# Kernel optimization log

Measured on AMD Instinct MI355X. Metric: run time of the kernel, lower is better.

The kernel has to match this reference:

```python
import jax, jax.numpy as jnp
import numpy as np

B, CIN, COUT, KH, KW, H, W = 32, 64, 64, 3, 3, 128, 128
STRIDE = (1, 1)
PADDING = [(1, 1), (1, 1)]


def setup_inputs() -> dict:
    key = jax.random.key(0)
    k1, k2, k3, k4 = jax.random.split(key, 4)
    x = jax.random.normal(k1, (B, CIN, H, W), dtype=jnp.float32)
    cov = jax.random.uniform(k2, (B,), dtype=jnp.float32)
    # kaiming-normal fan_out init: std = sqrt(2 / (cout*kh*kw))
    std = np.sqrt(2.0 / (COUT * KH * KW)).astype(np.float32)
    W_0 = jax.random.normal(k3, (COUT, CIN, KH, KW), dtype=jnp.float32) * std
    W_1 = jax.random.normal(k4, (COUT, CIN, KH, KW), dtype=jnp.float32) * std
    return {"x": x, "cov": cov, "W_0": W_0, "W_1": W_1}


def reference(x, cov, W_0, W_1):
    # per-sample kernel: W_0 + cov[i] * W_1  -> [B, COUT, CIN, KH, KW]
    kernels = W_0[None] + cov[:, None, None, None, None] * W_1[None]

    def conv_one(xi, k):
        # xi: [CIN, H, W], k: [COUT, CIN, KH, KW]
        out = jax.lax.conv_general_dilated(
            xi[None], k, window_strides=STRIDE, padding=PADDING,
            dimension_numbers=("NCHW", "OIHW", "NCHW"))
        return out[0]

    return jax.vmap(conv_one)(x, kernels)  # [B, COUT, H, W]
```

## Files before the change

### kernel.cpp

```cpp
#include <hip/hip_runtime.h>
#include <stdint.h>

#define B_   32
#define CIN  64
#define COUT 64
#define H_   128
#define W_   128
#define WP   130
#define HW_  (H_ * W_)
#define SLOT (WP * 64)

typedef __bf16 bf16x8 __attribute__((ext_vector_type(8)));
typedef float  f32x4  __attribute__((ext_vector_type(4)));

__device__ inline unsigned int f2bf(float f) {
  union { float f; unsigned u; } uf; uf.f = f;
  unsigned u = uf.u;
  unsigned r = 0x7FFFu + ((u >> 16) & 1u);
  return (u + r) >> 16;
}

__device__ inline unsigned int pk2(float a, float b) {
  unsigned short x = __builtin_bit_cast(unsigned short, (__bf16)a);
  unsigned short y = __builtin_bit_cast(unsigned short, (__bf16)b);
  return (unsigned int)x | ((unsigned int)y << 16);
}

__global__ __launch_bounds__(256) void prep_w(const float* __restrict__ W0,
                                              const float* __restrict__ W1,
                                              const float* __restrict__ cov,
                                              unsigned short* __restrict__ Wb) {
  int g   = blockIdx.x * 256 + threadIdx.x;
  int j   = g & 7;
  int l   = (g >> 3) & 63;
  int cq4 = (g >> 9) & 3;
  int ck  = (g >> 11) & 1;
  int v   = g >> 12;
  int b   = v / 9;
  int p   = v - b * 9;
  int cout = cq4 * 16 + (l & 15);
  int ci   = ck * 32 + (l >> 4) * 8 + j;
  int widx = (cout * CIN + ci) * 9 + p;
  float val = W0[widx] + cov[b] * W1[widx];
  Wb[g] = (unsigned short)f2bf(val);
}

__global__ __launch_bounds__(1024, 4) void conv_strip(
    const float* __restrict__ X,
    const unsigned short* __restrict__ Wb,
    float* __restrict__ out) {
  __shared__ __align__(16) unsigned short Xs[6 * SLOT];

  int bid   = blockIdx.x;
  int b     = (bid & 7) * 4 + (bid >> 6);
  int strip = (bid >> 3) & 7;
  int h0    = strip * 16;

  int t  = threadIdx.x;
  int wv = t >> 6;
  int l  = t & 63;
  int lh = l & 15;
  int q  = l >> 4;

  int a = wv >> 3;
  int o = wv & 7;
  int cq4 = wv & 3;
  int pq  = wv >> 2;
  int rbase  = pq >> 1;
  int cbase0 = (pq & 1) * 64 + lh;

  int wp0 = 2 * l + 1, wp1 = 2 * l + 2;
  int sw0 = (o ^ (wp0 & 7)) << 3, sw1 = (o ^ (wp1 & 7)) << 3;

  if (wv < 6) {
    unsigned int* d32 = (unsigned int*)(Xs + wv * SLOT + (l < 32 ? 0 : 129 * 64));
    d32[l & 31] = 0u;
  }
  {
    int r  = wv >> 2;
    int ih = h0 - 1 + r;
    unsigned short* dr = Xs + r * SLOT;
    #pragma unroll
    for (int oi = 0; oi < 2; oi++) {
      int oo = (wv & 3) * 2 + oi;
      uint4 v0 = {0, 0, 0, 0}, v1 = {0, 0, 0, 0};
      if (ih >= 0) {
        const float* sp = X + ((size_t)(b * CIN + oo * 8) * H_ + ih) * W_ + 2 * l;
        float2 tt[8];
        #pragma unroll
        for (int j = 0; j < 8; j++) tt[j] = *(const float2*)(sp + (size_t)j * HW_);
        v0.x = pk2(tt[0].x, tt[1].x); v0.y = pk2(tt[2].x, tt[3].x);
        v0.z = pk2(tt[4].x, tt[5].x); v0.w = pk2(tt[6].x, tt[7].x);
        v1.x = pk2(tt[0].y, tt[1].y); v1.y = pk2(tt[2].y, tt[3].y);
        v1.z = pk2(tt[4].y, tt[5].y); v1.w = pk2(tt[6].y, tt[7].y);
      }
      *(uint4*)(dr + wp0 * 64 + ((oo ^ (wp0 & 7)) << 3)) = v0;
      *(uint4*)(dr + wp1 * 64 + ((oo ^ (wp1 & 7)) << 3)) = v1;
    }
  }
  __syncthreads();

  const unsigned short* wb9 = Wb + (size_t)b * 9 * 4096;

  float2 st[8];
  int sb = 0;

  #pragma unroll 1
  for (int k = 0; k < 8; k++) {
    if (k > 0) {
      int sw = sb + 2 + a; if (sw >= 6) sw -= 6;
      unsigned short* dr = Xs + sw * SLOT;
      uint4 v0, v1;
      v0.x = pk2(st[0].x, st[1].x); v0.y = pk2(st[2].x, st[3].x);
      v0.z = pk2(st[4].x, st[5].x); v0.w = pk2(st[6].x, st[7].x);
      v1.x = pk2(st[0].y, st[1].y); v1.y = pk2(st[2].y, st[3].y);
      v1.z = pk2(st[4].y, st[5].y); v1.w = pk2(st[6].y, st[7].y);
      *(uint4*)(dr + wp0 * 64 + sw0) = v0;
      *(uint4*)(dr + wp1 * 64 + sw1) = v1;
    }
    asm volatile("s_waitcnt lgkmcnt(0)" ::: "memory");
    __builtin_amdgcn_s_barrier();
    __builtin_amdgcn_sched_barrier(0);

    if (k < 7) {
      int ih = h0 + 2 * k + 3 + a;
      if (ih <= 127) {
        const float* sp = X + ((size_t)(b * CIN + o * 8) * H_ + ih) * W_ + 2 * l;
        #pragma unroll
        for (int j = 0; j < 8; j++) st[j] = *(const float2*)(sp + (size_t)j * HW_);
      } else {
        #pragma unroll
        for (int j = 0; j < 8; j++) st[j] = (float2){0.f, 0.f};
      }
    }
    __builtin_amdgcn_sched_barrier(0);

    f32x4 acc[4];
    #pragma unroll
    for (int nt = 0; nt < 4; nt++) acc[nt] = (f32x4){0.f, 0.f, 0.f, 0.f};

    #pragma unroll 1
    for (int kh = 0; kh < 3; kh++) {
      int r6 = sb + rbase + kh; if (r6 >= 6) r6 -= 6;
      const unsigned short* rp = Xs + r6 * SLOT;
      #pragma unroll
      for (int kw = 0; kw < 3; kw++) {
        const unsigned short* wk = wb9 + (kh * 3 + kw) * 4096;
        #pragma unroll
        for (int ck = 0; ck < 2; ck++) {
          bf16x8 af = *(const bf16x8*)(wk + (ck * 4 + cq4) * 512 + l * 8);
          bf16x8 bfr[4];
          #pragma unroll
          for (int nt = 0; nt < 4; nt++) {
            int c = cbase0 + nt * 16 + kw;
            int blk = (ck * 4 + q) ^ (c & 7);
            bfr[nt] = *(const bf16x8*)(rp + c * 64 + blk * 8);
          }
          __builtin_amdgcn_s_setprio(1);
          #pragma unroll
          for (int nt = 0; nt < 4; nt++)
            acc[nt] = __builtin_amdgcn_mfma_f32_16x16x32_bf16(
                af, bfr[nt], acc[nt], 0, 0, 0);
          __builtin_amdgcn_s_setprio(0);
        }
      }
    }

    int oh = h0 + 2 * k + rbase;
    #pragma unroll
    for (int nt = 0; nt < 4; nt++) {
      int ow = cbase0 + nt * 16;
      #pragma unroll
      for (int r = 0; r < 4; r++) {
        int cout = cq4 * 16 + q * 4 + r;
        out[(((size_t)b * COUT + cout) * H_ + oh) * W_ + ow] = acc[nt][r];
      }
    }

    sb += 2; if (sb >= 6) sb -= 6;
  }
}

extern "C" void kernel_launch(void* const* d_in, const int* in_sizes, int n_in,
                              void* d_out, int out_size, void* d_ws, size_t ws_size,
                              hipStream_t stream) {
  const float* x   = (const float*)d_in[0];
  const float* cov = (const float*)d_in[1];
  const float* W0  = (const float*)d_in[2];
  const float* W1  = (const float*)d_in[3];
  float* out = (float*)d_out;

  unsigned short* Wb = (unsigned short*)d_ws;

  prep_w    <<<dim3(4608), dim3(256),  0, stream>>>(W0, W1, cov, Wb);
  conv_strip<<<dim3(256),  dim3(1024), 0, stream>>>(x, Wb, out);
}
```

Measured before the change: 284.7 us.

## Switch conv inner product from 16x16x32 to 32x32x16 bf16 MFMA tiles

Each wave now computes a 32-cout by 32-pixel tile with the 32x32x16 bf16 MFMA instead of four 16x16x32 MFMAs over a 16-cout by 64-pixel tile. The weight prep kernel is relaid out to match the new A-fragment layout, and the output store mapping is changed to fit the 32x32 accumulator layout. The aim is higher MFMA throughput per instruction and fewer B-fragment LDS reads per MAC. In exchange, the accumulator is now sixteen registers per lane and each lane's stores touch more cout rows.

```diff
diff --git a/kernel.cpp b/kernel.cpp
--- a/kernel.cpp
+++ b/kernel.cpp
@@ -11,7 +11,7 @@
 #define SLOT (WP * 64)
 
 typedef __bf16 bf16x8 __attribute__((ext_vector_type(8)));
-typedef float  f32x4  __attribute__((ext_vector_type(4)));
+typedef float  f32x16 __attribute__((ext_vector_type(16)));
 
 __device__ inline unsigned int f2bf(float f) {
   union { float f; unsigned u; } uf; uf.f = f;
@@ -30,16 +30,16 @@
                                               const float* __restrict__ W1,
                                               const float* __restrict__ cov,
                                               unsigned short* __restrict__ Wb) {
-  int g   = blockIdx.x * 256 + threadIdx.x;
-  int j   = g & 7;
-  int l   = (g >> 3) & 63;
-  int cq4 = (g >> 9) & 3;
-  int ck  = (g >> 11) & 1;
-  int v   = g >> 12;
-  int b   = v / 9;
-  int p   = v - b * 9;
-  int cout = cq4 * 16 + (l & 15);
-  int ci   = ck * 32 + (l >> 4) * 8 + j;
+  int g    = blockIdx.x * 256 + threadIdx.x;
+  int j    = g & 7;
+  int l    = (g >> 3) & 63;
+  int ch   = (g >> 9) & 1;
+  int ck16 = (g >> 10) & 3;
+  int v    = g >> 12;
+  int b    = v / 9;
+  int p    = v - b * 9;
+  int cout = ch * 32 + (l & 31);
+  int ci   = ck16 * 16 + (l >> 5) * 8 + j;
   int widx = (cout * CIN + ci) * 9 + p;
   float val = W0[widx] + cov[b] * W1[widx];
   Wb[g] = (unsigned short)f2bf(val);
@@ -59,15 +59,14 @@
   int t  = threadIdx.x;
   int wv = t >> 6;
   int l  = t & 63;
-  int lh = l & 15;
-  int q  = l >> 4;
 
   int a = wv >> 3;
   int o = wv & 7;
-  int cq4 = wv & 3;
-  int pq  = wv >> 2;
-  int rbase  = pq >> 1;
-  int cbase0 = (pq & 1) * 64 + lh;
+  int ch = wv & 1;
+  int pq = wv >> 1;
+  int rbase = pq >> 2;
+  int cpix  = (pq & 3) * 32 + (l & 31);
+  int ohalf = l >> 5;
 
   int wp0 = 2 * l + 1, wp1 = 2 * l + 2;
   int sw0 = (o ^ (wp0 & 7)) << 3, sw1 = (o ^ (wp1 & 7)) << 3;
@@ -135,9 +134,9 @@
     }
     __builtin_amdgcn_sched_barrier(0);
 
-    f32x4 acc[4];
+    f32x16 acc;
     #pragma unroll
-    for (int nt = 0; nt < 4; nt++) acc[nt] = (f32x4){0.f, 0.f, 0.f, 0.f};
+    for (int i = 0; i < 16; i++) acc[i] = 0.f;
 
     #pragma unroll 1
     for (int kh = 0; kh < 3; kh++) {
@@ -145,35 +144,32 @@
       const unsigned short* rp = Xs + r6 * SLOT;
       #pragma unroll
       for (int kw = 0; kw < 3; kw++) {
-        const unsigned short* wk = wb9 + (kh * 3 + kw) * 4096;
+        const unsigned short* wk = wb9 + (size_t)((kh * 3 + kw) * 4 * 2 + ch) * 512;
+        int c = cpix + kw;
+        bf16x8 af[4], bfr[4];
         #pragma unroll
-        for (int ck = 0; ck < 2; ck++) {
-          bf16x8 af = *(const bf16x8*)(wk + (ck * 4 + cq4) * 512 + l * 8);
-          bf16x8 bfr[4];
-          #pragma unroll
-          for (int nt = 0; nt < 4; nt++) {
-            int c = cbase0 + nt * 16 + kw;
-            int blk = (ck * 4 + q) ^ (c & 7);
-            bfr[nt] = *(const bf16x8*)(rp + c * 64 + blk * 8);
-          }
-          __builtin_amdgcn_s_setprio(1);
-          #pragma unroll
-          for (int nt = 0; nt < 4; nt++)
-            acc[nt] = __builtin_amdgcn_mfma_f32_16x16x32_bf16(
-                af, bfr[nt], acc[nt], 0, 0, 0);
-          __builtin_amdgcn_s_setprio(0);
+        for (int ck = 0; ck < 4; ck++)
+          af[ck] = *(const bf16x8*)(wk + (size_t)ck * 1024 + l * 8);
+        #pragma unroll
+        for (int ck = 0; ck < 4; ck++) {
+          int blk = (2 * ck + ohalf) ^ (c & 7);
+          bfr[ck] = *(const bf16x8*)(rp + c * 64 + blk * 8);
         }
+        __builtin_amdgcn_s_setprio(1);
+        #pragma unroll
+        for (int ck = 0; ck < 4; ck++)
+          acc = __builtin_amdgcn_mfma_f32_32x32x16_bf16(af[ck], bfr[ck], acc, 0, 0, 0);
+        __builtin_amdgcn_s_setprio(0);
       }
     }
 
-    int oh = h0 + 2 * k + rbase;
-    #pragma unroll
-    for (int nt = 0; nt < 4; nt++) {
-      int ow = cbase0 + nt * 16;
+    {
+      int oh = h0 + 2 * k + rbase;
+      size_t obase = (((size_t)b * COUT + ch * 32 + 4 * ohalf) * H_ + oh) * W_ + cpix;
       #pragma unroll
-      for (int r = 0; r < 4; r++) {
-        int cout = cq4 * 16 + q * 4 + r;
-        out[(((size_t)b * COUT + cout) * H_ + oh) * W_ + ow] = acc[nt][r];
+      for (int reg = 0; reg < 16; reg++) {
+        int coff = (reg & 3) + 8 * (reg >> 2);
+        out[obase + (size_t)coff * HW_] = acc[reg];
       }
     }
 
```

New measurement: 288.4 us. About the same (+1.3%).
